# Performance work log

Measured on AMD Instinct MI355X. Metric: run time of the kernel, lower is better.

## Reference

```python
import jax, jax.numpy as jnp
import numpy as np

D = 256   # input_size
H = 512   # hidden_size
A = 4     # alpha_dim
K = 2 * A * A  # output values per input dim (binary=False -> 2 params)


def _masks():
    # MADE sequential-ordering masks, per DART.create_masks
    in_deg = np.arange(D)
    hid_deg = np.arange(H) % (D - 1)
    out_deg = np.arange(D) - 1  # arange(D) % D - 1
    m0 = (hid_deg[:, None] >= in_deg[None, :]).astype(np.float32)   # [H, D]
    mh = (hid_deg[:, None] >= hid_deg[None, :]).astype(np.float32)  # [H, H]
    ml = (out_deg[:, None] >= hid_deg[None, :]).astype(np.float32)  # [D, H]
    # repeat(1, K).view(-1, H): each output-dim row repeated K consecutive times
    ml = np.repeat(ml, K, axis=0)                                    # [D*K, H]
    return jnp.asarray(m0), jnp.asarray(mh), jnp.asarray(ml)


def setup_inputs() -> dict:
    key = jax.random.key(0)
    ks = jax.random.split(key, 10)
    B = 1024
    x = jax.random.normal(ks[0], (B, D), dtype=jnp.float32)
    def lin(k, out_dim, in_dim):
        s = 1.0 / np.sqrt(in_dim)
        kw, kb = jax.random.split(k)
        W = jax.random.uniform(kw, (out_dim, in_dim), jnp.float32, -s, s)
        b = jax.random.uniform(kb, (out_dim,), jnp.float32, -s, s)
        return W, b
    W0, b0 = lin(ks[1], H, D)
    W1, b1 = lin(ks[2], H, H)
    W2, b2 = lin(ks[3], H, H)
    Wout, bout = lin(ks[4], D * K, H)
    # unnormalized_log_p_alpha initialized to log(1/A)
    ulpa = jnp.full((1, D - 1, 1, A), -np.log(A), dtype=jnp.float32)
    return {"x": x, "W0": W0, "b0": b0, "W1": W1, "b1": b1,
            "W2": W2, "b2": b2, "Wout": Wout, "bout": bout, "ulpa": ulpa}


def reference(x, W0, b0, W1, b1, W2, b2, Wout, bout, ulpa):
    m0, mh, ml = _masks()
    B = x.shape[0]
    # masked MLP (MADE)
    h = jax.nn.relu(x @ (m0 * W0).T + b0)
    h = jax.nn.relu(h @ (mh * W1).T + b1)
    h = jax.nn.relu(h @ (mh * W2).T + b2)
    theta = (h @ (ml * Wout).T + bout).reshape(B, D, 2, A, A)
    mu = theta[:, :, 0]                      # [B, D, A, A]
    std = jnp.exp(theta[:, :, 1]) + 0.01     # [B, D, A, A]
    xe = x[:, :, None, None]
    # Normal log-prob
    log_px = -0.5 * jnp.square((xe - mu) / std) - jnp.log(std) - 0.5 * jnp.log(2.0 * jnp.pi)
    # normalized log p(alpha): [1, D-1, 1, A]
    lpa = jax.nn.log_softmax(ulpa, axis=-1)
    joint = log_px[:, :-1] + lpa             # [B, D-1, A, A]
    first = joint[:, 0, 0:1]                 # [B, 1, A]
    inner = jnp.swapaxes(joint[:, 1:], 0, 1)  # [D-2, B, A, A]
    # HMM-style forward recursion: stable log-domain chain matmul via scan
    def step(carry, m):
        # carry: [B, 1, A]; m: [B, A, A]
        new = jax.nn.logsumexp(carry[:, :, :, None] + m[:, None, :, :], axis=-2)
        return new, None
    carry, _ = jax.lax.scan(step, first, inner)
    last = log_px[:, -1, :, 0:1]             # [B, A, 1]
    log_p = jax.nn.logsumexp(carry[:, :, :, None] + last[:, None, :, :], axis=-2)  # [B,1,1]
    return log_p, theta
```

## Files before the change

### kernel.cpp

```cpp
#include <hip/hip_runtime.h>
#include <math.h>

#define Bsz 1024
#define Dd  256
#define Hh  512
#define NOUT 8192

typedef __attribute__((ext_vector_type(8))) short bf8_t;
typedef __attribute__((ext_vector_type(4))) float f4_t;

__device__ inline ushort f2b(float f) {
  union { float f; unsigned u; } c; c.f = f;
  unsigned r = c.u + 0x7fffu + ((c.u >> 16) & 1u);
  return (ushort)(r >> 16);
}

__device__ inline void async16(const ushort* g, ushort* l) {
  __builtin_amdgcn_global_load_lds((const __attribute__((address_space(1))) void*)g,
                                   (__attribute__((address_space(3))) void*)l, 16, 0, 0);
}

__device__ inline int mod255(int v) {
  if (v >= 510) return v - 510;
  if (v >= 255) return v - 255;
  return v;
}

__global__ __launch_bounds__(256) void prep(
    const float* __restrict__ x,  const float* __restrict__ W0,
    const float* __restrict__ W1, const float* __restrict__ W2,
    const float* __restrict__ Wout,
    ushort* __restrict__ xb, ushort* __restrict__ w0b, ushort* __restrict__ w1b,
    ushort* __restrict__ w2b, ushort* __restrict__ woutb)
{
  const int blk = blockIdx.x, tid = threadIdx.x;
  const float* src; ushort* dst; int lb, mode;
  if (blk < 128)      { src = x;    dst = xb;    lb = blk;       mode = 0; }
  else if (blk < 192) { src = W0;   dst = w0b;   lb = blk - 128; mode = 1; }
  else if (blk < 320) { src = W1;   dst = w1b;   lb = blk - 192; mode = 2; }
  else if (blk < 448) { src = W2;   dst = w2b;   lb = blk - 320; mode = 2; }
  else                { src = Wout; dst = woutb; lb = blk - 448; mode = 3; }

  const int e = lb * 2048 + tid * 8;
  float4 v0 = *(const float4*)(src + e);
  float4 v1 = *(const float4*)(src + e + 4);
  float vv[8] = {v0.x, v0.y, v0.z, v0.w, v1.x, v1.y, v1.z, v1.w};
  ushort u[8];
  if (mode == 0) {
#pragma unroll
    for (int i = 0; i < 8; i++) u[i] = f2b(vv[i]);
  } else if (mode == 1) {
    int n = e >> 8, k0 = e & 255, nd = mod255(n);
#pragma unroll
    for (int i = 0; i < 8; i++) u[i] = (nd >= k0 + i) ? f2b(vv[i]) : (ushort)0;
  } else if (mode == 2) {
    int n = e >> 9, k0 = e & 511, nd = mod255(n);
#pragma unroll
    for (int i = 0; i < 8; i++) u[i] = (nd >= mod255(k0 + i)) ? f2b(vv[i]) : (ushort)0;
  } else {
    int n = e >> 9, k0 = e & 511, nd = (n >> 5) - 1;
#pragma unroll
    for (int i = 0; i < 8; i++) u[i] = (nd >= mod255(k0 + i)) ? f2b(vv[i]) : (ushort)0;
  }
  *(ushort4*)(dst + e)     = *(ushort4*)&u[0];
  *(ushort4*)(dst + e + 4) = *(ushort4*)&u[4];
}

template<int BM, int BN, int RELU, int OUTF32>
__global__ __launch_bounds__(256) void gemm_bf(
    const ushort* __restrict__ A, const ushort* __restrict__ W,
    const float* __restrict__ bias, float* __restrict__ Cf, ushort* __restrict__ Ch,
    int M, int N, int Kd)
{
  constexpr int WM = BM / 2, WN = BN / 2, MI = WM / 16, NI = WN / 16;
  __shared__ ushort As[BM * 64];
  __shared__ ushort Bs[BN * 64];
  const int tid = threadIdx.x, lane = tid & 63, wave = tid >> 6;
  const int waveM = wave >> 1, waveN = wave & 1;
  const int row0 = blockIdx.y * BM, col0 = blockIdx.x * BN;
  const int fm = lane & 15, qq = lane >> 4;
  const int srow = lane >> 3, qslot = lane & 7;

  f4_t acc[MI][NI];
#pragma unroll
  for (int i = 0; i < MI; i++)
#pragma unroll
    for (int j = 0; j < NI; j++) acc[i][j] = (f4_t){0.f, 0.f, 0.f, 0.f};

  for (int kt = 0; kt < Kd; kt += 64) {
#pragma unroll
    for (int p = 0; p < BM / 32; p++) {
      int rb = p * 32 + wave * 8;
      int r = rb + srow;
      int q = (qslot - r) & 7;
      const ushort* g = A + (size_t)(row0 + r) * Kd + kt + q * 8;
      async16(g, &As[rb * 64]);
    }
#pragma unroll
    for (int p = 0; p < BN / 32; p++) {
      int rb = p * 32 + wave * 8;
      int r = rb + srow;
      int q = (qslot - r) & 7;
      const ushort* g = W + (size_t)(col0 + r) * Kd + kt + q * 8;
      async16(g, &Bs[rb * 64]);
    }
    __syncthreads();

#pragma unroll
    for (int t = 0; t < 2; t++) {
      bf8_t af[MI], bf[NI];
#pragma unroll
      for (int i = 0; i < MI; i++) {
        int r = waveM * WM + i * 16 + fm;
        int slot = ((t * 4 + qq) + r) & 7;
        af[i] = *(const bf8_t*)&As[r * 64 + slot * 8];
      }
#pragma unroll
      for (int j = 0; j < NI; j++) {
        int r = waveN * WN + j * 16 + fm;
        int slot = ((t * 4 + qq) + r) & 7;
        bf[j] = *(const bf8_t*)&Bs[r * 64 + slot * 8];
      }
#pragma unroll
      for (int i = 0; i < MI; i++)
#pragma unroll
        for (int j = 0; j < NI; j++)
          acc[i][j] = __builtin_amdgcn_mfma_f32_16x16x32_bf16(af[i], bf[j], acc[i][j], 0, 0, 0);
    }
    __syncthreads();
  }

#pragma unroll
  for (int j = 0; j < NI; j++) {
    int col = col0 + waveN * WN + j * 16 + fm;
    float bv = bias[col];
#pragma unroll
    for (int i = 0; i < MI; i++) {
      int rbase = row0 + waveM * WM + i * 16 + qq * 4;
#pragma unroll
      for (int r = 0; r < 4; r++) {
        float t = acc[i][j][r] + bv;
        if (RELU) t = fmaxf(t, 0.0f);
        if (OUTF32) Cf[(size_t)(rbase + r) * N + col] = t;
        else        Ch[(size_t)(rbase + r) * N + col] = f2b(t);
      }
    }
  }
}

__global__ void lpa_kernel(const float* __restrict__ ulpa, float* __restrict__ lpa)
{
  int d = blockIdx.x * blockDim.x + threadIdx.x;
  if (d < Dd - 1) {
    float v0 = ulpa[d * 4 + 0], v1 = ulpa[d * 4 + 1];
    float v2 = ulpa[d * 4 + 2], v3 = ulpa[d * 4 + 3];
    float m = fmaxf(fmaxf(v0, v1), fmaxf(v2, v3));
    float s = __expf(v0 - m) + __expf(v1 - m) + __expf(v2 - m) + __expf(v3 - m);
    float l = m + __logf(s);
    lpa[d * 4 + 0] = v0 - l;
    lpa[d * 4 + 1] = v1 - l;
    lpa[d * 4 + 2] = v2 - l;
    lpa[d * 4 + 3] = v3 - l;
  }
}

__global__ __launch_bounds__(256) void chain2(
    const float* __restrict__ x, const float* __restrict__ theta,
    const float* __restrict__ lpa, float* __restrict__ logp)
{
  const int b = blockIdx.x;
  const int tid = threadIdx.x;
  const int seg = tid >> 4, e = tid & 15;
  const int i = e >> 2, jj = e & 3;
  const int base = (tid & 63) & ~15;
  const float C0 = 0.91893853320467274178f;
  const float* th = theta + (size_t)b * NOUT;
  const float* xb = x + (size_t)b * Dd;
  __shared__ float Ts[16][16];

  const int d0 = 1 + seg * 16;
  const int d1 = min(d0 + 16, Dd - 1);

  auto stepm = [&](int d) -> float {
    float mu = th[d * 32 + e];
    float ls = th[d * 32 + 16 + e];
    float s  = __expf(ls) + 0.01f;
    float z  = (xb[d] - mu) * __builtin_amdgcn_rcpf(s);
    return -0.5f * z * z - __logf(s) - C0 + lpa[d * 4 + jj];
  };

  float T = stepm(d0);
  for (int d = d0 + 1; d < d1; d++) {
    float m_ = stepm(d);
    float v0 = __shfl(T, base + i * 4 + 0) + __shfl(m_, base + 0 * 4 + jj);
    float v1 = __shfl(T, base + i * 4 + 1) + __shfl(m_, base + 1 * 4 + jj);
    float v2 = __shfl(T, base + i * 4 + 2) + __shfl(m_, base + 2 * 4 + jj);
    float v3 = __shfl(T, base + i * 4 + 3) + __shfl(m_, base + 3 * 4 + jj);
    float mx = fmaxf(fmaxf(v0, v1), fmaxf(v2, v3));
    float s  = __expf(v0 - mx) + __expf(v1 - mx) + __expf(v2 - mx) + __expf(v3 - mx);
    T = mx + __logf(s);
  }
  Ts[seg][e] = T;
  __syncthreads();

  if (tid < 4) {
    const int j = tid;
    float mu = th[j], ls = th[16 + j];
    float s = __expf(ls) + 0.01f;
    float z = (xb[0] - mu) * __builtin_amdgcn_rcpf(s);
    float carry = -0.5f * z * z - __logf(s) - C0 + lpa[j];
#pragma unroll 1
    for (int sg = 0; sg < 16; sg++) {
      float c0 = __shfl(carry, 0);
      float c1 = __shfl(carry, 1);
      float c2 = __shfl(carry, 2);
      float c3 = __shfl(carry, 3);
      float v0 = c0 + Ts[sg][0 * 4 + j];
      float v1 = c1 + Ts[sg][1 * 4 + j];
      float v2 = c2 + Ts[sg][2 * 4 + j];
      float v3 = c3 + Ts[sg][3 * 4 + j];
      float mx = fmaxf(fmaxf(v0, v1), fmaxf(v2, v3));
      float ss = __expf(v0 - mx) + __expf(v1 - mx) + __expf(v2 - mx) + __expf(v3 - mx);
      carry = mx + __logf(ss);
    }
    float mu2 = th[255 * 32 + j * 4], ls2 = th[255 * 32 + 16 + j * 4];
    float s2 = __expf(ls2) + 0.01f;
    float z2 = (xb[255] - mu2) * __builtin_amdgcn_rcpf(s2);
    float v = carry - 0.5f * z2 * z2 - __logf(s2) - C0;
    float mx = fmaxf(v, __shfl_xor(v, 1));
    mx = fmaxf(mx, __shfl_xor(mx, 2));
    float ee = __expf(v - mx);
    ee += __shfl_xor(ee, 1);
    ee += __shfl_xor(ee, 2);
    if (j == 0) logp[b] = mx + __logf(ee);
  }
}

extern "C" void kernel_launch(void* const* d_in, const int* in_sizes, int n_in,
                              void* d_out, int out_size, void* d_ws, size_t ws_size,
                              hipStream_t stream)
{
  const float* x    = (const float*)d_in[0];
  const float* W0   = (const float*)d_in[1];
  const float* b0   = (const float*)d_in[2];
  const float* W1   = (const float*)d_in[3];
  const float* b1   = (const float*)d_in[4];
  const float* W2   = (const float*)d_in[5];
  const float* b2   = (const float*)d_in[6];
  const float* Wout = (const float*)d_in[7];
  const float* bout = (const float*)d_in[8];
  const float* ulpa = (const float*)d_in[9];

  float* out   = (float*)d_out;
  float* logp  = out;
  float* theta = out + Bsz;

  ushort* ws    = (ushort*)d_ws;
  ushort* xb    = ws;
  ushort* w0b   = xb + 262144;
  ushort* w1b   = w0b + 131072;
  ushort* w2b   = w1b + 262144;
  ushort* woutb = w2b + 262144;
  ushort* h0    = woutb + 4194304;
  ushort* h1    = h0 + 524288;
  ushort* h2    = h0;
  float*  lpa   = (float*)(h1 + 524288);

  prep<<<2496, 256, 0, stream>>>(x, W0, W1, W2, Wout, xb, w0b, w1b, w2b, woutb);
  lpa_kernel<<<1, 256, 0, stream>>>(ulpa, lpa);
  gemm_bf<64, 64, 1, 0><<<dim3(Hh / 64, Bsz / 64), 256, 0, stream>>>(xb, w0b, b0, nullptr, h0, Bsz, Hh, Dd);
  gemm_bf<64, 64, 1, 0><<<dim3(Hh / 64, Bsz / 64), 256, 0, stream>>>(h0, w1b, b1, nullptr, h1, Bsz, Hh, Hh);
  gemm_bf<64, 64, 1, 0><<<dim3(Hh / 64, Bsz / 64), 256, 0, stream>>>(h1, w2b, b2, nullptr, h2, Bsz, Hh, Hh);
  gemm_bf<128, 128, 0, 1><<<dim3(NOUT / 128, Bsz / 128), 256, 0, stream>>>(h2, woutb, bout, theta, nullptr, Bsz, NOUT, Hh);
  chain2<<<Bsz, 256, 0, stream>>>(x, theta, lpa, logp);
}
```

Measured before the change: 144.8 us.

## Fuse three hidden-layer GEMMs into one persistent kernel with grid barriers

The log-softmax of ulpa moves into an extra block of the prep kernel, which also zeroes a barrier counter. The three 64x64-tile hidden-layer GEMM launches are merged into a single 128-block kernel that uses an atomic grid-wide barrier between layers, so h2 gets its own buffer. The aim is to remove kernel launch and drain gaps between small dependent kernels. The barrier relies on all 128 blocks being co-resident, and spin-waiting adds its own synchronisation cost.

```diff
diff --git a/kernel.cpp b/kernel.cpp
--- a/kernel.cpp
+++ b/kernel.cpp
@@ -29,11 +29,27 @@
 __global__ __launch_bounds__(256) void prep(
     const float* __restrict__ x,  const float* __restrict__ W0,
     const float* __restrict__ W1, const float* __restrict__ W2,
-    const float* __restrict__ Wout,
+    const float* __restrict__ Wout, const float* __restrict__ ulpa,
     ushort* __restrict__ xb, ushort* __restrict__ w0b, ushort* __restrict__ w1b,
-    ushort* __restrict__ w2b, ushort* __restrict__ woutb)
+    ushort* __restrict__ w2b, ushort* __restrict__ woutb,
+    float* __restrict__ lpa, unsigned* __restrict__ bar)
 {
   const int blk = blockIdx.x, tid = threadIdx.x;
+  if (blk == 2496) {
+    if (tid < 16) bar[tid] = 0u;
+    if (tid < Dd - 1) {
+      float v0 = ulpa[tid * 4 + 0], v1 = ulpa[tid * 4 + 1];
+      float v2 = ulpa[tid * 4 + 2], v3 = ulpa[tid * 4 + 3];
+      float m = fmaxf(fmaxf(v0, v1), fmaxf(v2, v3));
+      float s = __expf(v0 - m) + __expf(v1 - m) + __expf(v2 - m) + __expf(v3 - m);
+      float l = m + __logf(s);
+      lpa[tid * 4 + 0] = v0 - l;
+      lpa[tid * 4 + 1] = v1 - l;
+      lpa[tid * 4 + 2] = v2 - l;
+      lpa[tid * 4 + 3] = v3 - l;
+    }
+    return;
+  }
   const float* src; ushort* dst; int lb, mode;
   if (blk < 128)      { src = x;    dst = xb;    lb = blk;       mode = 0; }
   else if (blk < 192) { src = W0;   dst = w0b;   lb = blk - 128; mode = 1; }
@@ -66,101 +82,179 @@
   *(ushort4*)(dst + e + 4) = *(ushort4*)&u[4];
 }
 
-template<int BM, int BN, int RELU, int OUTF32>
-__global__ __launch_bounds__(256) void gemm_bf(
+__device__ inline void gridbar(unsigned* bar, unsigned target) {
+  __syncthreads();
+  if (threadIdx.x == 0) {
+    __threadfence();
+    __hip_atomic_fetch_add(bar, 1u, __ATOMIC_ACQ_REL, __HIP_MEMORY_SCOPE_AGENT);
+    while (__hip_atomic_load(bar, __ATOMIC_ACQUIRE, __HIP_MEMORY_SCOPE_AGENT) < target) {}
+  }
+  __syncthreads();
+  __threadfence();
+}
+
+__device__ __forceinline__ void tile_gemm64(
     const ushort* __restrict__ A, const ushort* __restrict__ W,
-    const float* __restrict__ bias, float* __restrict__ Cf, ushort* __restrict__ Ch,
-    int M, int N, int Kd)
-{
-  constexpr int WM = BM / 2, WN = BN / 2, MI = WM / 16, NI = WN / 16;
-  __shared__ ushort As[BM * 64];
-  __shared__ ushort Bs[BN * 64];
+    const float* __restrict__ bias, ushort* __restrict__ Ch,
+    int N, int Kd, int row0, int col0, ushort* As, ushort* Bs)
+{
   const int tid = threadIdx.x, lane = tid & 63, wave = tid >> 6;
   const int waveM = wave >> 1, waveN = wave & 1;
-  const int row0 = blockIdx.y * BM, col0 = blockIdx.x * BN;
   const int fm = lane & 15, qq = lane >> 4;
   const int srow = lane >> 3, qslot = lane & 7;
 
-  f4_t acc[MI][NI];
-#pragma unroll
-  for (int i = 0; i < MI; i++)
-#pragma unroll
-    for (int j = 0; j < NI; j++) acc[i][j] = (f4_t){0.f, 0.f, 0.f, 0.f};
+  f4_t acc[2][2];
+#pragma unroll
+  for (int i = 0; i < 2; i++)
+#pragma unroll
+    for (int j = 0; j < 2; j++) acc[i][j] = (f4_t){0.f, 0.f, 0.f, 0.f};
 
   for (int kt = 0; kt < Kd; kt += 64) {
 #pragma unroll
-    for (int p = 0; p < BM / 32; p++) {
+    for (int p = 0; p < 2; p++) {
       int rb = p * 32 + wave * 8;
       int r = rb + srow;
       int q = (qslot - r) & 7;
-      const ushort* g = A + (size_t)(row0 + r) * Kd + kt + q * 8;
-      async16(g, &As[rb * 64]);
-    }
-#pragma unroll
-    for (int p = 0; p < BN / 32; p++) {
+      async16(A + (size_t)(row0 + r) * Kd + kt + q * 8, &As[rb * 64]);
+    }
+#pragma unroll
+    for (int p = 0; p < 2; p++) {
       int rb = p * 32 + wave * 8;
       int r = rb + srow;
       int q = (qslot - r) & 7;
-      const ushort* g = W + (size_t)(col0 + r) * Kd + kt + q * 8;
-      async16(g, &Bs[rb * 64]);
+      async16(W + (size_t)(col0 + r) * Kd + kt + q * 8, &Bs[rb * 64]);
     }
     __syncthreads();
-
 #pragma unroll
     for (int t = 0; t < 2; t++) {
-      bf8_t af[MI], bf[NI];
-#pragma unroll
-      for (int i = 0; i < MI; i++) {
-        int r = waveM * WM + i * 16 + fm;
+      bf8_t af[2], bf[2];
+#pragma unroll
+      for (int i = 0; i < 2; i++) {
+        int r = waveM * 32 + i * 16 + fm;
         int slot = ((t * 4 + qq) + r) & 7;
         af[i] = *(const bf8_t*)&As[r * 64 + slot * 8];
       }
 #pragma unroll
-      for (int j = 0; j < NI; j++) {
-        int r = waveN * WN + j * 16 + fm;
+      for (int j = 0; j < 2; j++) {
+        int r = waveN * 32 + j * 16 + fm;
         int slot = ((t * 4 + qq) + r) & 7;
         bf[j] = *(const bf8_t*)&Bs[r * 64 + slot * 8];
       }
 #pragma unroll
-      for (int i = 0; i < MI; i++)
-#pragma unroll
-        for (int j = 0; j < NI; j++)
+      for (int i = 0; i < 2; i++)
+#pragma unroll
+        for (int j = 0; j < 2; j++)
           acc[i][j] = __builtin_amdgcn_mfma_f32_16x16x32_bf16(af[i], bf[j], acc[i][j], 0, 0, 0);
     }
     __syncthreads();
   }
 
 #pragma unroll
-  for (int j = 0; j < NI; j++) {
-    int col = col0 + waveN * WN + j * 16 + fm;
+  for (int j = 0; j < 2; j++) {
+    int col = col0 + waveN * 32 + j * 16 + fm;
     float bv = bias[col];
 #pragma unroll
-    for (int i = 0; i < MI; i++) {
-      int rbase = row0 + waveM * WM + i * 16 + qq * 4;
+    for (int i = 0; i < 2; i++) {
+      int rbase = row0 + waveM * 32 + i * 16 + qq * 4;
 #pragma unroll
       for (int r = 0; r < 4; r++) {
-        float t = acc[i][j][r] + bv;
-        if (RELU) t = fmaxf(t, 0.0f);
-        if (OUTF32) Cf[(size_t)(rbase + r) * N + col] = t;
-        else        Ch[(size_t)(rbase + r) * N + col] = f2b(t);
-      }
-    }
-  }
-}
-
-__global__ void lpa_kernel(const float* __restrict__ ulpa, float* __restrict__ lpa)
-{
-  int d = blockIdx.x * blockDim.x + threadIdx.x;
-  if (d < Dd - 1) {
-    float v0 = ulpa[d * 4 + 0], v1 = ulpa[d * 4 + 1];
-    float v2 = ulpa[d * 4 + 2], v3 = ulpa[d * 4 + 3];
-    float m = fmaxf(fmaxf(v0, v1), fmaxf(v2, v3));
-    float s = __expf(v0 - m) + __expf(v1 - m) + __expf(v2 - m) + __expf(v3 - m);
-    float l = m + __logf(s);
-    lpa[d * 4 + 0] = v0 - l;
-    lpa[d * 4 + 1] = v1 - l;
-    lpa[d * 4 + 2] = v2 - l;
-    lpa[d * 4 + 3] = v3 - l;
+        float t = fmaxf(acc[i][j][r] + bv, 0.0f);
+        Ch[(size_t)(rbase + r) * N + col] = f2b(t);
+      }
+    }
+  }
+}
+
+__global__ __launch_bounds__(256) void mlp3(
+    const ushort* __restrict__ xb,
+    const ushort* __restrict__ w0b, const float* __restrict__ b0,
+    const ushort* __restrict__ w1b, const float* __restrict__ b1,
+    const ushort* __restrict__ w2b, const float* __restrict__ b2,
+    ushort* __restrict__ h0, ushort* __restrict__ h1, ushort* __restrict__ h2,
+    unsigned* __restrict__ bar)
+{
+  __shared__ ushort As[64 * 64];
+  __shared__ ushort Bs[64 * 64];
+  const int row0 = (blockIdx.x >> 3) * 64;
+  const int col0 = (blockIdx.x & 7) * 64;
+
+  tile_gemm64(xb, w0b, b0, h0, Hh, Dd, row0, col0, As, Bs);
+  gridbar(bar, 128);
+  tile_gemm64(h0, w1b, b1, h1, Hh, Hh, row0, col0, As, Bs);
+  gridbar(bar, 256);
+  tile_gemm64(h1, w2b, b2, h2, Hh, Hh, row0, col0, As, Bs);
+}
+
+__global__ __launch_bounds__(256) void gemm_big(
+    const ushort* __restrict__ A, const ushort* __restrict__ W,
+    const float* __restrict__ bias, float* __restrict__ Cf,
+    int M, int N, int Kd)
+{
+  __shared__ ushort As[128 * 64];
+  __shared__ ushort Bs[128 * 64];
+  const int tid = threadIdx.x, lane = tid & 63, wave = tid >> 6;
+  const int waveM = wave >> 1, waveN = wave & 1;
+  const int row0 = blockIdx.y * 128, col0 = blockIdx.x * 128;
+  const int fm = lane & 15, qq = lane >> 4;
+  const int srow = lane >> 3, qslot = lane & 7;
+
+  f4_t acc[4][4];
+#pragma unroll
+  for (int i = 0; i < 4; i++)
+#pragma unroll
+    for (int j = 0; j < 4; j++) acc[i][j] = (f4_t){0.f, 0.f, 0.f, 0.f};
+
+  for (int kt = 0; kt < Kd; kt += 64) {
+#pragma unroll
+    for (int p = 0; p < 4; p++) {
+      int rb = p * 32 + wave * 8;
+      int r = rb + srow;
+      int q = (qslot - r) & 7;
+      async16(A + (size_t)(row0 + r) * Kd + kt + q * 8, &As[rb * 64]);
+    }
+#pragma unroll
+    for (int p = 0; p < 4; p++) {
+      int rb = p * 32 + wave * 8;
+      int r = rb + srow;
+      int q = (qslot - r) & 7;
+      async16(W + (size_t)(col0 + r) * Kd + kt + q * 8, &Bs[rb * 64]);
+    }
+    __syncthreads();
+#pragma unroll
+    for (int t = 0; t < 2; t++) {
+      bf8_t af[4], bf[4];
+#pragma unroll
+      for (int i = 0; i < 4; i++) {
+        int r = waveM * 64 + i * 16 + fm;
+        int slot = ((t * 4 + qq) + r) & 7;
+        af[i] = *(const bf8_t*)&As[r * 64 + slot * 8];
+      }
+#pragma unroll
+      for (int j = 0; j < 4; j++) {
+        int r = waveN * 64 + j * 16 + fm;
+        int slot = ((t * 4 + qq) + r) & 7;
+        bf[j] = *(const bf8_t*)&Bs[r * 64 + slot * 8];
+      }
+#pragma unroll
+      for (int i = 0; i < 4; i++)
+#pragma unroll
+        for (int j = 0; j < 4; j++)
+          acc[i][j] = __builtin_amdgcn_mfma_f32_16x16x32_bf16(af[i], bf[j], acc[i][j], 0, 0, 0);
+    }
+    __syncthreads();
+  }
+
+#pragma unroll
+  for (int j = 0; j < 4; j++) {
+    int col = col0 + waveN * 64 + j * 16 + fm;
+    float bv = bias[col];
+#pragma unroll
+    for (int i = 0; i < 4; i++) {
+      int rbase = row0 + waveM * 64 + i * 16 + qq * 4;
+#pragma unroll
+      for (int r = 0; r < 4; r++)
+        Cf[(size_t)(rbase + r) * N + col] = acc[i][j][r] + bv;
+    }
   }
 }
 
@@ -263,14 +357,13 @@
   ushort* woutb = w2b + 262144;
   ushort* h0    = woutb + 4194304;
   ushort* h1    = h0 + 524288;
-  ushort* h2    = h0;
-  float*  lpa   = (float*)(h1 + 524288);
-
-  prep<<<2496, 256, 0, stream>>>(x, W0, W1, W2, Wout, xb, w0b, w1b, w2b, woutb);
-  lpa_kernel<<<1, 256, 0, stream>>>(ulpa, lpa);
-  gemm_bf<64, 64, 1, 0><<<dim3(Hh / 64, Bsz / 64), 256, 0, stream>>>(xb, w0b, b0, nullptr, h0, Bsz, Hh, Dd);
-  gemm_bf<64, 64, 1, 0><<<dim3(Hh / 64, Bsz / 64), 256, 0, stream>>>(h0, w1b, b1, nullptr, h1, Bsz, Hh, Hh);
-  gemm_bf<64, 64, 1, 0><<<dim3(Hh / 64, Bsz / 64), 256, 0, stream>>>(h1, w2b, b2, nullptr, h2, Bsz, Hh, Hh);
-  gemm_bf<128, 128, 0, 1><<<dim3(NOUT / 128, Bsz / 128), 256, 0, stream>>>(h2, woutb, bout, theta, nullptr, Bsz, NOUT, Hh);
+  ushort* h2    = h1 + 524288;
+  float*  lpa   = (float*)(h2 + 524288);
+  unsigned* bar = (unsigned*)(lpa + 1024);
+
+  prep<<<2497, 256, 0, stream>>>(x, W0, W1, W2, Wout, ulpa,
+                                 xb, w0b, w1b, w2b, woutb, lpa, bar);
+  mlp3<<<128, 256, 0, stream>>>(xb, w0b, b0, w1b, b1, w2b, b2, h0, h1, h2, bar);
+  gemm_big<<<dim3(NOUT / 128, Bsz / 128), 256, 0, stream>>>(h2, woutb, bout, theta, Bsz, NOUT, Hh);
   chain2<<<Bsz, 256, 0, stream>>>(x, theta, lpa, logp);
 }
```

Result: slower. 166.5 us (+14.9%).
